# Kernel tuning notes

Hardware: AMD Instinct MI355X
Metric: run time of the kernel (lower is better)

The kernel has to match this reference:

```python
import jax, jax.numpy as jnp
import numpy as np

TEMPERATURE = 0.1
EPS = 1e-08
NEG_INF = -9e15


def setup_inputs() -> dict:
    key = jax.random.key(0)
    k1, k2 = jax.random.split(key)
    B, D = 4096, 256
    z_i = jax.random.normal(k1, (B, D), dtype=jnp.float32)
    z_j = jax.random.normal(k2, (B, D), dtype=jnp.float32)
    mask_positive = jnp.ones((B,), dtype=bool)
    return {"z_i": z_i, "z_j": z_j, "mask_positive": mask_positive}


def reference(z_i, z_j, mask_positive):
    B = z_i.shape[0]
    N = 2 * B
    z = jnp.concatenate([z_i, z_j], axis=0)  # [N, D]
    # cosine similarity: normalize (norms clamped to eps) then GEMM
    norms = jnp.maximum(jnp.linalg.norm(z, axis=1, keepdims=True), EPS)
    zn = z / norms
    sim = jnp.matmul(zn, zn.T) / TEMPERATURE  # [N, N]
    # mask self-similarity on diagonal
    rows = jnp.arange(N)
    sim = sim.at[rows, rows].set(NEG_INF)
    logprob = jax.nn.log_softmax(sim, axis=1)
    # positive of row k is row (k+B) mod N
    positives = jnp.concatenate([jnp.arange(B, N), jnp.arange(0, B)])
    loss_vec = -logprob[rows, positives]  # [N]
    mp = jnp.concatenate([mask_positive, mask_positive])  # [N] bool
    cnt = jnp.sum(mp.astype(jnp.float32))
    total = jnp.sum(jnp.where(mp, loss_vec, 0.0))
    loss = jnp.where(cnt > 0, total / jnp.maximum(cnt, 1.0), 0.0)
    return loss
```

## Files before the change

kernel.cpp:

```cpp
#include <hip/hip_runtime.h>
#include <hip/hip_bf16.h>

#define NTOT   8192
#define BHALF  4096
#define DDIM   256
#define NPART  4
#define EXPSCALE 14.4269504088896341f

typedef __attribute__((ext_vector_type(8))) short bf16x8_t;
typedef __attribute__((ext_vector_type(4))) float f32x4_t;

__device__ inline unsigned short f2bf(float x) {
    __hip_bfloat16 h = __float2bfloat16(x);
    return __builtin_bit_cast(unsigned short, h);
}

__global__ void norm_pair_kernel(const float* __restrict__ zi,
                                 const float* __restrict__ zj,
                                 unsigned short* __restrict__ zn,
                                 float* __restrict__ posdot,
                                 float* __restrict__ s_part) {
    int gtid = blockIdx.x * 256 + threadIdx.x;
    if (gtid < NTOT * NPART) s_part[gtid] = 0.0f;
    int k    = gtid >> 6;
    int lane = gtid & 63;
    float4 vi = reinterpret_cast<const float4*>(zi + (size_t)k * DDIM)[lane];
    float4 vj = reinterpret_cast<const float4*>(zj + (size_t)k * DDIM)[lane];
    float ssi = vi.x*vi.x + vi.y*vi.y + vi.z*vi.z + vi.w*vi.w;
    float ssj = vj.x*vj.x + vj.y*vj.y + vj.z*vj.z + vj.w*vj.w;
    float dot = vi.x*vj.x + vi.y*vj.y + vi.z*vj.z + vi.w*vj.w;
    #pragma unroll
    for (int off = 32; off >= 1; off >>= 1) {
        ssi += __shfl_xor(ssi, off);
        ssj += __shfl_xor(ssj, off);
        dot += __shfl_xor(dot, off);
    }
    float ri = 1.0f / fmaxf(sqrtf(ssi), 1e-8f);
    float rj = 1.0f / fmaxf(sqrtf(ssj), 1e-8f);
    ushort4 oi, oj;
    oi.x = f2bf(vi.x * ri); oi.y = f2bf(vi.y * ri);
    oi.z = f2bf(vi.z * ri); oi.w = f2bf(vi.w * ri);
    oj.x = f2bf(vj.x * rj); oj.y = f2bf(vj.y * rj);
    oj.z = f2bf(vj.z * rj); oj.w = f2bf(vj.w * rj);
    reinterpret_cast<ushort4*>(zn + (size_t)k * DDIM)[lane] = oi;
    reinterpret_cast<ushort4*>(zn + (size_t)(k + BHALF) * DDIM)[lane] = oj;
    if (lane == 0) posdot[k] = dot * ri * rj * 10.0f;
}

__global__ void __launch_bounds__(256)
gemm_kernel(const unsigned short* __restrict__ zn,
            float* __restrict__ s_part) {
    __shared__ unsigned short ldsB[64 * 256];

    const int tid  = threadIdx.x;
    const int lane = tid & 63;
    const int wv   = tid >> 6;
    const int m    = lane & 15;
    const int quad = lane >> 4;
    const int bi   = blockIdx.x;
    const int s    = blockIdx.y;
    const int R0   = bi << 7;
    const int CB   = s << 9;

    float* rowPart = s_part + (size_t)(s & (NPART - 1)) * NTOT;

    bf16x8_t afrag[2][8];
    #pragma unroll
    for (int rf = 0; rf < 2; ++rf) {
        const unsigned short* arow = zn + (size_t)(R0 + wv*32 + rf*16 + m) * DDIM;
        #pragma unroll
        for (int kk = 0; kk < 8; ++kk)
            afrag[rf][kk] = *reinterpret_cast<const bf16x8_t*>(arow + kk*32 + quad*8);
    }

    bf16x8_t pf[8];
    #pragma unroll
    for (int t = 0; t < 8; ++t) {
        int ci = t * 256 + tid;
        int r = ci >> 5, c = ci & 31;
        pf[t] = *reinterpret_cast<const bf16x8_t*>(zn + (size_t)(CB + r) * DDIM + c * 8);
    }

    float rowacc[2][4] = {{0.f,0.f,0.f,0.f},{0.f,0.f,0.f,0.f}};

    for (int it = 0; it < 8; ++it) {
        const int C0 = CB + it * 64;
        const bool isDiag = ((C0 >> 7) == bi);

        __syncthreads();
        #pragma unroll
        for (int t = 0; t < 8; ++t) {
            int ci = t * 256 + tid;
            int r = ci >> 5, c = ci & 31;
            *reinterpret_cast<bf16x8_t*>(&ldsB[r * 256 + ((c ^ (r & 7)) << 3)]) = pf[t];
        }
        __syncthreads();

        if (it < 7) {
            #pragma unroll
            for (int t = 0; t < 8; ++t) {
                int ci = t * 256 + tid;
                int r = ci >> 5, c = ci & 31;
                pf[t] = *reinterpret_cast<const bf16x8_t*>(
                            zn + (size_t)(C0 + 64 + r) * DDIM + c * 8);
            }
        }

        #pragma unroll
        for (int cf = 0; cf < 4; ++cf) {
            f32x4_t c0 = (f32x4_t){0.f,0.f,0.f,0.f};
            f32x4_t c1 = (f32x4_t){0.f,0.f,0.f,0.f};
            #pragma unroll
            for (int kk = 0; kk < 8; ++kk) {
                bf16x8_t b = *reinterpret_cast<const bf16x8_t*>(
                    &ldsB[(cf*16 + m) * 256 + (((kk*4 + quad) ^ (m & 7)) << 3)]);
                c0 = __builtin_amdgcn_mfma_f32_16x16x32_bf16(afrag[0][kk], b, c0, 0, 0, 0);
                c1 = __builtin_amdgcn_mfma_f32_16x16x32_bf16(afrag[1][kk], b, c1, 0, 0, 0);
            }
            const int gc = C0 + cf*16 + m;
            #pragma unroll
            for (int r = 0; r < 4; ++r) {
                int gr0 = R0 + wv*32 + quad*4 + r;
                float e0 = exp2f(c0[r] * EXPSCALE);
                float e1 = exp2f(c1[r] * EXPSCALE);
                if (isDiag && gr0 == gc)        e0 = 0.f;
                if (isDiag && (gr0 + 16) == gc) e1 = 0.f;
                rowacc[0][r] += e0;
                rowacc[1][r] += e1;
            }
        }
    }

    #pragma unroll
    for (int rf = 0; rf < 2; ++rf)
        #pragma unroll
        for (int r = 0; r < 4; ++r) {
            float v = rowacc[rf][r];
            v += __shfl_xor(v, 1);
            v += __shfl_xor(v, 2);
            v += __shfl_xor(v, 4);
            v += __shfl_xor(v, 8);
            if (m == 0)
                atomicAdd(&rowPart[R0 + wv*32 + rf*16 + quad*4 + r], v);
        }
}

__global__ void finalize_kernel(const float* __restrict__ s_part,
                                const float* __restrict__ posdot,
                                const unsigned char* __restrict__ mask,
                                float* __restrict__ out) {
    int tid = threadIdx.x, lane = tid & 63, wv = tid >> 6;
    float tot = 0.f, cnt = 0.f;
    #pragma unroll
    for (int si = 0; si < NTOT / 1024; ++si) {
        int k = si * 1024 + tid;
        int kb = k & (BHALF - 1);
        if (mask[kb] != 0) {
            float sk = s_part[k] + s_part[NTOT + k]
                     + s_part[2*NTOT + k] + s_part[3*NTOT + k];
            tot += __logf(sk) - posdot[kb];
            cnt += 1.f;
        }
    }
    #pragma unroll
    for (int off = 32; off >= 1; off >>= 1) {
        tot += __shfl_xor(tot, off);
        cnt += __shfl_xor(cnt, off);
    }
    __shared__ float st[16], sc[16];
    if (lane == 0) { st[wv] = tot; sc[wv] = cnt; }
    __syncthreads();
    if (tid == 0) {
        float T = 0.f, C = 0.f;
        #pragma unroll
        for (int i = 0; i < 16; ++i) { T += st[i]; C += sc[i]; }
        out[0] = (C > 0.f) ? (T / fmaxf(C, 1.f)) : 0.f;
    }
}

extern "C" void kernel_launch(void* const* d_in, const int* in_sizes, int n_in,
                              void* d_out, int out_size, void* d_ws, size_t ws_size,
                              hipStream_t stream) {
    const float* zi = (const float*)d_in[0];
    const float* zj = (const float*)d_in[1];
    const unsigned char* mask = (const unsigned char*)d_in[2];
    float* out = (float*)d_out;

    unsigned short* zn = (unsigned short*)d_ws;
    float* s_part = (float*)((char*)d_ws + (size_t)NTOT * DDIM * 2);
    float* posdot = s_part + NPART * NTOT;

    norm_pair_kernel<<<dim3(1024), dim3(256), 0, stream>>>(zi, zj, zn, posdot, s_part);
    gemm_kernel<<<dim3(64, 16), dim3(256), 0, stream>>>(zn, s_part);
    finalize_kernel<<<dim3(1), dim3(1024), 0, stream>>>(s_part, posdot, mask, out);
}
```

Measured before the change: 119.3 us.

## Double row tile per block to reuse LDS B tiles across more MFMAs

Each block now covers 256 rows instead of 128, and each wave holds four 16-row A fragments, so every B fragment read from LDS feeds four MFMAs instead of two. The grid is halved to 32x16 blocks and launch bounds are set to (256,1). The diagonal masking is split into a separate branch so off-diagonal tiles skip the compare. The cost is more registers per thread and only 512 blocks, which lowers occupancy and may underfill the GPU.

```diff
diff --git a/kernel.cpp b/kernel.cpp
--- a/kernel.cpp
+++ b/kernel.cpp
@@ -47,7 +47,7 @@
     if (lane == 0) posdot[k] = dot * ri * rj * 10.0f;
 }
 
-__global__ void __launch_bounds__(256)
+__global__ void __launch_bounds__(256, 1)
 gemm_kernel(const unsigned short* __restrict__ zn,
             float* __restrict__ s_part) {
     __shared__ unsigned short ldsB[64 * 256];
@@ -59,80 +59,91 @@
     const int quad = lane >> 4;
     const int bi   = blockIdx.x;
     const int s    = blockIdx.y;
-    const int R0   = bi << 7;
+    const int R0   = bi << 8;
     const int CB   = s << 9;
 
     float* rowPart = s_part + (size_t)(s & (NPART - 1)) * NTOT;
 
-    bf16x8_t afrag[2][8];
-    #pragma unroll
-    for (int rf = 0; rf < 2; ++rf) {
-        const unsigned short* arow = zn + (size_t)(R0 + wv*32 + rf*16 + m) * DDIM;
+    bf16x8_t afrag[4][8];
+    #pragma unroll
+    for (int rf = 0; rf < 4; ++rf) {
+        const unsigned short* arow = zn + (size_t)(R0 + wv*64 + rf*16 + m) * DDIM;
         #pragma unroll
         for (int kk = 0; kk < 8; ++kk)
             afrag[rf][kk] = *reinterpret_cast<const bf16x8_t*>(arow + kk*32 + quad*8);
     }
 
     bf16x8_t pf[8];
-    #pragma unroll
-    for (int t = 0; t < 8; ++t) {
-        int ci = t * 256 + tid;
-        int r = ci >> 5, c = ci & 31;
-        pf[t] = *reinterpret_cast<const bf16x8_t*>(zn + (size_t)(CB + r) * DDIM + c * 8);
-    }
-
-    float rowacc[2][4] = {{0.f,0.f,0.f,0.f},{0.f,0.f,0.f,0.f}};
+    {
+        const int c = tid & 31, r0 = tid >> 5;
+        #pragma unroll
+        for (int t = 0; t < 8; ++t)
+            pf[t] = *reinterpret_cast<const bf16x8_t*>(
+                        zn + (size_t)(CB + t*8 + r0) * DDIM + c * 8);
+    }
+
+    float rowacc[4][4] = {{0.f,0.f,0.f,0.f},{0.f,0.f,0.f,0.f},
+                          {0.f,0.f,0.f,0.f},{0.f,0.f,0.f,0.f}};
 
     for (int it = 0; it < 8; ++it) {
         const int C0 = CB + it * 64;
-        const bool isDiag = ((C0 >> 7) == bi);
+        const bool isDiag = ((C0 >> 8) == bi);
 
         __syncthreads();
-        #pragma unroll
-        for (int t = 0; t < 8; ++t) {
-            int ci = t * 256 + tid;
-            int r = ci >> 5, c = ci & 31;
-            *reinterpret_cast<bf16x8_t*>(&ldsB[r * 256 + ((c ^ (r & 7)) << 3)]) = pf[t];
+        {
+            const int c = tid & 31, r0 = tid >> 5;
+            #pragma unroll
+            for (int t = 0; t < 8; ++t) {
+                int r = t*8 + r0;
+                *reinterpret_cast<bf16x8_t*>(&ldsB[r * 256 + ((c ^ (r & 7)) << 3)]) = pf[t];
+            }
         }
         __syncthreads();
 
         if (it < 7) {
-            #pragma unroll
-            for (int t = 0; t < 8; ++t) {
-                int ci = t * 256 + tid;
-                int r = ci >> 5, c = ci & 31;
+            const int c = tid & 31, r0 = tid >> 5;
+            #pragma unroll
+            for (int t = 0; t < 8; ++t)
                 pf[t] = *reinterpret_cast<const bf16x8_t*>(
-                            zn + (size_t)(C0 + 64 + r) * DDIM + c * 8);
-            }
+                            zn + (size_t)(C0 + 64 + t*8 + r0) * DDIM + c * 8);
         }
 
         #pragma unroll
         for (int cf = 0; cf < 4; ++cf) {
-            f32x4_t c0 = (f32x4_t){0.f,0.f,0.f,0.f};
-            f32x4_t c1 = (f32x4_t){0.f,0.f,0.f,0.f};
+            f32x4_t cacc[4];
+            #pragma unroll
+            for (int rf = 0; rf < 4; ++rf) cacc[rf] = (f32x4_t){0.f,0.f,0.f,0.f};
             #pragma unroll
             for (int kk = 0; kk < 8; ++kk) {
                 bf16x8_t b = *reinterpret_cast<const bf16x8_t*>(
                     &ldsB[(cf*16 + m) * 256 + (((kk*4 + quad) ^ (m & 7)) << 3)]);
-                c0 = __builtin_amdgcn_mfma_f32_16x16x32_bf16(afrag[0][kk], b, c0, 0, 0, 0);
-                c1 = __builtin_amdgcn_mfma_f32_16x16x32_bf16(afrag[1][kk], b, c1, 0, 0, 0);
+                #pragma unroll
+                for (int rf = 0; rf < 4; ++rf)
+                    cacc[rf] = __builtin_amdgcn_mfma_f32_16x16x32_bf16(
+                        afrag[rf][kk], b, cacc[rf], 0, 0, 0);
             }
             const int gc = C0 + cf*16 + m;
-            #pragma unroll
-            for (int r = 0; r < 4; ++r) {
-                int gr0 = R0 + wv*32 + quad*4 + r;
-                float e0 = exp2f(c0[r] * EXPSCALE);
-                float e1 = exp2f(c1[r] * EXPSCALE);
-                if (isDiag && gr0 == gc)        e0 = 0.f;
-                if (isDiag && (gr0 + 16) == gc) e1 = 0.f;
-                rowacc[0][r] += e0;
-                rowacc[1][r] += e1;
+            if (isDiag) {
+                #pragma unroll
+                for (int rf = 0; rf < 4; ++rf)
+                    #pragma unroll
+                    for (int r = 0; r < 4; ++r) {
+                        int gr = R0 + wv*64 + rf*16 + quad*4 + r;
+                        float e = exp2f(cacc[rf][r] * EXPSCALE);
+                        rowacc[rf][r] += (gr == gc) ? 0.f : e;
+                    }
+            } else {
+                #pragma unroll
+                for (int rf = 0; rf < 4; ++rf)
+                    #pragma unroll
+                    for (int r = 0; r < 4; ++r)
+                        rowacc[rf][r] += exp2f(cacc[rf][r] * EXPSCALE);
             }
         }
     }
 
     #pragma unroll
-    for (int rf = 0; rf < 2; ++rf)
+    for (int rf = 0; rf < 4; ++rf)
         #pragma unroll
         for (int r = 0; r < 4; ++r) {
             float v = rowacc[rf][r];
@@ -141,7 +152,7 @@
             v += __shfl_xor(v, 4);
             v += __shfl_xor(v, 8);
             if (m == 0)
-                atomicAdd(&rowPart[R0 + wv*32 + rf*16 + quad*4 + r], v);
+                atomicAdd(&rowPart[R0 + wv*64 + rf*16 + quad*4 + r], v);
         }
 }
 
@@ -191,6 +202,6 @@
     float* posdot = s_part + NPART * NTOT;
 
     norm_pair_kernel<<<dim3(1024), dim3(256), 0, stream>>>(zi, zj, zn, posdot, s_part);
-    gemm_kernel<<<dim3(64, 16), dim3(256), 0, stream>>>(zn, s_part);
+    gemm_kernel<<<dim3(32, 16), dim3(256), 0, stream>>>(zn, s_part);
     finalize_kernel<<<dim3(1), dim3(1024), 0, stream>>>(s_part, posdot, mask, out);
 }
```

Measured after the change: 126.0 us. 5.7% more time.
